# Optimization experiments

Hardware: AMD Instinct MI355X
Metric: run time of the kernel (lower is better)

Reference implementation:

```python
import jax, jax.numpy as jnp
import numpy as np

N, E, C, H, DE, B = 50000, 400000, 64, 4, 16, 64
EPS = 1e-5
NEG_SLOPE = 0.2
NBLOCKS = 2


def setup_inputs() -> dict:
    key = jax.random.key(0)
    ks = jax.random.split(key, 8)
    x = jax.random.normal(ks[0], (N, C), jnp.float32)
    edge_index = jax.random.randint(ks[1], (2, E), 0, N, dtype=jnp.int64)
    edge_attr = jax.random.normal(ks[2], (E, DE), jnp.float32)
    batch = jnp.sort(jax.random.randint(ks[3], (N,), 0, B, dtype=jnp.int64))
    s = 1.0 / np.sqrt(C)
    # stacked params for the 2 blocks
    Wl = jax.random.normal(ks[4], (NBLOCKS, C, H * C), jnp.float32) * s
    Wr = jax.random.normal(ks[5], (NBLOCKS, C, H * C), jnp.float32) * s
    We = jax.random.normal(ks[6], (NBLOCKS, DE, H * C), jnp.float32) * (1.0 / np.sqrt(DE))
    att = jax.random.normal(ks[7], (NBLOCKS, H, C), jnp.float32) * s
    gat_bias = jnp.zeros((NBLOCKS, C), jnp.float32)
    gn_weight = jnp.ones((NBLOCKS, C), jnp.float32)
    gn_bias = jnp.zeros((NBLOCKS, C), jnp.float32)
    gn_mean_scale = jnp.ones((NBLOCKS, C), jnp.float32)
    return dict(x=x, edge_index=edge_index, edge_attr=edge_attr, batch=batch,
                Wl=Wl, Wr=Wr, We=We, att=att, gat_bias=gat_bias,
                gn_weight=gn_weight, gn_bias=gn_bias, gn_mean_scale=gn_mean_scale)


def _segment_mean(v, seg, num):
    s = jax.ops.segment_sum(v, seg, num_segments=num)
    cnt = jax.ops.segment_sum(jnp.ones((v.shape[0], 1), v.dtype), seg, num_segments=num)
    return s / jnp.maximum(cnt, 1.0)


def _graph_norm(x, batch, w, b, ms):
    mean = _segment_mean(x, batch, B)                 # [B, C]
    sub = x - ms * mean[batch]
    var = _segment_mean(sub * sub, batch, B)          # [B, C]
    return sub / jnp.sqrt(var[batch] + EPS) * w + b


def _gatv2(x, src, dst, ea, Wl, Wr, We, att, bias):
    # src/dst/ea already include self loops (E2 = E + N edges)
    xl = (x @ Wl).reshape(N, H, C)                    # source transform
    xr = (x @ Wr).reshape(N, H, C)                    # target transform
    ee = (ea @ We).reshape(-1, H, C)                  # [E2, H, C]
    f = jax.nn.leaky_relu(xl[src] + xr[dst] + ee, NEG_SLOPE)
    logits = jnp.einsum('ehc,hc->eh', f, att)         # [E2, H]
    m = jax.ops.segment_max(logits, dst, num_segments=N)
    a = jnp.exp(logits - m[dst])
    denom = jax.ops.segment_sum(a, dst, num_segments=N)
    alpha = a / denom[dst]                            # per-target softmax
    out = jax.ops.segment_sum(xl[src] * alpha[:, :, None], dst, num_segments=N)
    return out.mean(axis=1) + bias                    # concat=False -> head mean


def reference(x, edge_index, edge_attr, batch, Wl, Wr, We, att, gat_bias,
              gn_weight, gn_bias, gn_mean_scale):
    loop = jnp.arange(N, dtype=edge_index.dtype)
    src = jnp.concatenate([edge_index[0], loop])
    dst = jnp.concatenate([edge_index[1], loop])
    # add_self_loops with fill_value='mean'
    ea = jnp.concatenate([edge_attr,
                          jnp.broadcast_to(edge_attr.mean(axis=0), (N, DE))])
    residual = x
    for i in range(NBLOCKS):
        h = _graph_norm(x, batch, gn_weight[i], gn_bias[i], gn_mean_scale[i])
        h = jax.nn.relu(h)
        x = _gatv2(h, src, dst, ea, Wl[i], Wr[i], We[i], att[i], gat_bias[i])
    return x + residual
```

## Files before the change

### kernel.cpp

```cpp
#include <hip/hip_runtime.h>
#include <math.h>

#define NN 50000
#define EE 400000
#define ETOT 450000
#define CC 64
#define HH 4
#define DEA 16
#define NBATCH 64
#define HC 256
#define EPSV 1e-5f
#define NB 49
#define NGB 782
#define NPW 2
#define HISTB 1758
#define PACKB 128

typedef unsigned short ushort_t;
typedef unsigned int uint_t;
using h2t = decltype(__builtin_amdgcn_cvt_pkrtz(0.0f, 0.0f));

__device__ __forceinline__ float4 ld4(const float* p){ return *(const float4*)p; }
__device__ __forceinline__ int rfl(int v){ return __builtin_amdgcn_readfirstlane(v); }
__device__ __forceinline__ ushort_t f2b(float f){
  uint_t u = __float_as_uint(f);
  uint_t r = (u + 0x7FFFu + ((u >> 16) & 1u)) >> 16;
  return (ushort_t)r;
}
__device__ __forceinline__ float b2f_lo(uint_t u){ return __uint_as_float(u << 16); }
__device__ __forceinline__ float b2f_hi(uint_t u){ return __uint_as_float(u & 0xFFFF0000u); }
__device__ __forceinline__ uint_t h2u(h2t h){ return __builtin_bit_cast(uint_t, h); }
__device__ __forceinline__ h2t u2h(uint_t u){ return __builtin_bit_cast(h2t, u); }

template<int CTRL>
__device__ __forceinline__ float dpp_add(float x){
  int y = __builtin_amdgcn_update_dpp(0, __float_as_int(x), CTRL, 0xF, 0xF, true);
  return x + __int_as_float(y);
}
__device__ __forceinline__ float red16(float x){
  x = dpp_add<0xB1>(x);
  x = dpp_add<0x4E>(x);
  x = dpp_add<0x141>(x);
  x = dpp_add<0x140>(x);
  return x;
}

__global__ __launch_bounds__(256)
void k_pre1(const float* __restrict__ ea, const int* __restrict__ dst,
            float* __restrict__ easum, int* __restrict__ cnt){
  int tid = threadIdx.x;
  int bid = blockIdx.x;
  int e = bid*256 + tid;
  if (e < ETOT){
    int d = (e < EE) ? dst[e] : (e - EE);
    atomicAdd(&cnt[d], 1);
  }
  if (bid < 1024){
    int gid = bid*256 + tid;
    const int gsz = 262144;
    float s = 0.f;
    for (long long i = gid; i < (long long)EE*DEA; i += gsz) s += ea[i];
    __shared__ float sd[256];
    sd[tid] = s; __syncthreads();
    if (tid < DEA){
      float t = 0.f;
      for (int j = tid; j < 256; j += DEA) t += sd[j];
      atomicAdd(&easum[tid], t);
    }
  }
}

__global__ __launch_bounds__(1024)
void k_scan1(const int* __restrict__ cnt, int* __restrict__ loc, int* __restrict__ bsum){
  __shared__ int wsum[16];
  int tid = threadIdx.x, lane = tid & 63, wv = tid >> 6;
  int i = blockIdx.x*1024 + tid;
  int v = (i < NN) ? cnt[i] : 0;
  int incl = v;
  #pragma unroll
  for (int off = 1; off < 64; off <<= 1){
    int t = __shfl_up(incl, off, 64);
    if (lane >= off) incl += t;
  }
  if (lane == 63) wsum[wv] = incl;
  __syncthreads();
  if (wv == 0){
    int s = (lane < 16) ? wsum[lane] : 0;
    #pragma unroll
    for (int off = 1; off < 16; off <<= 1){
      int t = __shfl_up(s, off, 64);
      if (lane >= off) s += t;
    }
    if (lane < 16) wsum[lane] = s;
  }
  __syncthreads();
  int excl = (wv ? wsum[wv-1] : 0) + incl - v;
  if (i < NN) loc[i] = excl;
  if (tid == 1023) bsum[blockIdx.x] = wsum[15];
}

__global__ void k_scan2(int* __restrict__ bsum, int* __restrict__ row_ptr){
  int lane = threadIdx.x;
  int v = (lane < NB) ? bsum[lane] : 0;
  int incl = v;
  #pragma unroll
  for (int off = 1; off < 64; off <<= 1){
    int t = __shfl_up(incl, off, 64);
    if (lane >= off) incl += t;
  }
  if (lane < NB) bsum[lane] = incl - v;
  if (lane == 63) row_ptr[NN] = incl;
}

__global__ __launch_bounds__(1024)
void k_scan3(const int* __restrict__ loc, const int* __restrict__ bsum,
             int* __restrict__ row_ptr, int* __restrict__ wp){
  int i = blockIdx.x*1024 + threadIdx.x;
  if (i < NN){
    int v = loc[i] + bsum[blockIdx.x];
    row_ptr[i] = v; wp[i] = v;
  }
}

__global__ __launch_bounds__(256)
void k_pre2(const int* __restrict__ dst, const int* __restrict__ src,
            const float* __restrict__ ea, const float* __restrict__ easum,
            int* __restrict__ wp, int* __restrict__ csrc, uint_t* __restrict__ eas,
            const float* __restrict__ Wl, const float* __restrict__ Wr,
            uint_t* __restrict__ Wq){
  int bid = blockIdx.x;
  int tid = threadIdx.x;
  if (bid < HISTB){
    int e = bid*256 + tid;
    if (e >= ETOT) return;
    int d, s;
    if (e < EE){ d = dst[e]; s = src[e]; } else { d = e - EE; s = d; }
    int pos = atomicAdd(&wp[d], 1);
    csrc[pos] = s;
    float buf[16];
    if (e < EE){
      #pragma unroll
      for (int q = 0; q < 4; q++){
        float4 v = ld4(ea + (size_t)e*DEA + q*4);
        buf[q*4+0]=v.x; buf[q*4+1]=v.y; buf[q*4+2]=v.z; buf[q*4+3]=v.w;
      }
    } else {
      const float invE = 1.0f / (float)EE;
      #pragma unroll
      for (int k = 0; k < 16; k++) buf[k] = easum[k]*invE;
    }
    uint_t pk[8];
    #pragma unroll
    for (int p = 0; p < 8; p++)
      pk[p] = h2u(__builtin_amdgcn_cvt_pkrtz(buf[2*p], buf[2*p+1]));
    *(uint4*)(eas + (size_t)pos*8 + 0) = make_uint4(pk[0], pk[1], pk[2], pk[3]);
    *(uint4*)(eas + (size_t)pos*8 + 4) = make_uint4(pk[4], pk[5], pk[6], pk[7]);
  } else {
    int t = (bid - HISTB)*256 + tid;
    int col = t & 255;
    int kp  = (t >> 8) & 31;
    int lm  = t >> 13;
    int l = lm >> 1, mat = lm & 1;
    const float* W = (mat ? Wr : Wl) + (size_t)l*CC*HC;
    float w0 = W[(size_t)(2*kp+0)*HC + col];
    float w1 = W[(size_t)(2*kp+1)*HC + col];
    Wq[(size_t)lm*8192 + kp*256 + col] = h2u(__builtin_amdgcn_cvt_pkrtz(w0, w1));
  }
}

__global__ __launch_bounds__(256)
void k_stats(const float* __restrict__ x, const int* __restrict__ batch,
             float* __restrict__ S, float* __restrict__ Q){
  int c = threadIdx.x & 63, g = threadIdx.x >> 6;
  int r0 = blockIdx.x*256;
  int hiR = r0 + 256; if (hiR > NN) hiR = NN;
  float s = 0.f, q = 0.f;
  int curb = -1;
  for (int n = r0 + g; n < hiR; n += 4){
    int b = batch[n];
    if (b != curb){
      if (curb >= 0){ atomicAdd(&S[curb*64+c], s); atomicAdd(&Q[curb*64+c], q); }
      curb = b; s = 0.f; q = 0.f;
    }
    float v = x[(size_t)n*CC + c];
    s += v; q += v*v;
  }
  if (curb >= 0){ atomicAdd(&S[curb*64+c], s); atomicAdd(&Q[curb*64+c], q); }
}

__device__ __forceinline__ int lowerb(const int* a, int n, int key){
  int lo = 0, hi = n;
  while (lo < hi){ int mid = (lo+hi) >> 1; if (a[mid] < key) lo = mid+1; else hi = mid; }
  return lo;
}

__global__ void k_fin(const float* __restrict__ S, const float* __restrict__ Q,
                      const int* __restrict__ batch,
                      const float* __restrict__ w, const float* __restrict__ bb,
                      const float* __restrict__ ms,
                      float* __restrict__ scale, float* __restrict__ shift){
  __shared__ float cntf;
  int b = blockIdx.x, c = threadIdx.x;
  if (c == 0){
    int lo = lowerb(batch, NN, b), hi = lowerb(batch, NN, b+1);
    cntf = fmaxf((float)(hi - lo), 1.f);
  }
  __syncthreads();
  float inv = 1.f / cntf;
  float m = S[b*64+c] * inv;
  float a = ms[c] * m;
  float var = Q[b*64+c]*inv - 2.f*a*m + a*a;
  var = fmaxf(var, 0.f);
  float rstd = rsqrtf(var + EPSV);
  float sc = rstd * w[c];
  scale[b*64+c] = sc;
  shift[b*64+c] = bb[c] - a*sc;
}

__global__ __launch_bounds__(256)
void k_gemm(const float* __restrict__ x, const int* __restrict__ batch,
            const float* __restrict__ scale, const float* __restrict__ shift,
            const uint_t* __restrict__ WqA, const uint_t* __restrict__ WqB,
            ushort_t* __restrict__ outA, ushort_t* __restrict__ outB){
  const uint_t* Wq = blockIdx.z ? WqB : WqA;
  ushort_t* out = blockIdx.z ? outB : outA;
  int n0 = blockIdx.x * 64;
  __shared__ uint_t hTp[32][72];
  int tid = threadIdx.x;
  for (int t = tid; t < 1024; t += 256){
    int r = t >> 4, ch = t & 15;
    int n = n0 + r;
    float4 v = make_float4(0.f,0.f,0.f,0.f);
    if (n < NN){
      int b = batch[n];
      v = ld4(x + (size_t)n*CC + ch*4);
      float4 sc = ld4(scale + b*64 + ch*4);
      float4 sh = ld4(shift + b*64 + ch*4);
      v.x = fmaxf(v.x*sc.x + sh.x, 0.f);
      v.y = fmaxf(v.y*sc.y + sh.y, 0.f);
      v.z = fmaxf(v.z*sc.z + sh.z, 0.f);
      v.w = fmaxf(v.w*sc.w + sh.w, 0.f);
    }
    hTp[ch*2+0][r] = h2u(__builtin_amdgcn_cvt_pkrtz(v.x, v.y));
    hTp[ch*2+1][r] = h2u(__builtin_amdgcn_cvt_pkrtz(v.z, v.w));
  }
  __syncthreads();
  int c = tid & 63, rg = tid >> 6;
  int r0 = rg * 16;
  float acc[16][4];
  #pragma unroll
  for (int i = 0; i < 16; i++){ acc[i][0]=0.f; acc[i][1]=0.f; acc[i][2]=0.f; acc[i][3]=0.f; }
  #pragma unroll 4
  for (int kp = 0; kp < 32; kp++){
    uint4 a0 = *(const uint4*)&hTp[kp][r0+0];
    uint4 a1 = *(const uint4*)&hTp[kp][r0+4];
    uint4 a2 = *(const uint4*)&hTp[kp][r0+8];
    uint4 a3 = *(const uint4*)&hTp[kp][r0+12];
    uint4 wv = *(const uint4*)(Wq + (size_t)kp*256 + c*4);
    h2t w0 = u2h(wv.x), w1 = u2h(wv.y), w2 = u2h(wv.z), w3 = u2h(wv.w);
    const uint_t av[16] = {a0.x,a0.y,a0.z,a0.w, a1.x,a1.y,a1.z,a1.w,
                           a2.x,a2.y,a2.z,a2.w, a3.x,a3.y,a3.z,a3.w};
    #pragma unroll
    for (int i = 0; i < 16; i++){
      h2t e = u2h(av[i]);
      acc[i][0] = __builtin_amdgcn_fdot2(e, w0, acc[i][0], false);
      acc[i][1] = __builtin_amdgcn_fdot2(e, w1, acc[i][1], false);
      acc[i][2] = __builtin_amdgcn_fdot2(e, w2, acc[i][2], false);
      acc[i][3] = __builtin_amdgcn_fdot2(e, w3, acc[i][3], false);
    }
  }
  #pragma unroll
  for (int i = 0; i < 16; i++){
    int n = n0 + r0 + i;
    if (n < NN){
      uint2 o;
      o.x = (uint_t)f2b(acc[i][0]) | ((uint_t)f2b(acc[i][1]) << 16);
      o.y = (uint_t)f2b(acc[i][2]) | ((uint_t)f2b(acc[i][3]) << 16);
      *(uint2*)(out + (size_t)n*HC + c*4) = o;
    }
  }
}

__global__ __launch_bounds__(256, 4)
void k_gat(const int* __restrict__ row_ptr, const int* __restrict__ csrc,
           const uint_t* __restrict__ eas,
           const ushort_t* __restrict__ xlh, const ushort_t* __restrict__ xrh,
           const float* __restrict__ We, const float* __restrict__ att,
           const float* __restrict__ bias, const float* __restrict__ resid,
           float* __restrict__ out){
  int lane = threadIdx.x & 63;
  int h = lane >> 4, cg = lane & 15;
  int col = h*64 + cg*4;
  int wid = (blockIdx.x*256 + threadIdx.x) >> 6;
  int n0 = wid * NPW;
  if (n0 >= NN) return;
  int n1 = n0 + NPW; if (n1 > NN) n1 = NN;

  uint_t werh[4][8];
  #pragma unroll
  for (int p = 0; p < 8; p++){
    float4 w0 = ld4(We + (size_t)(2*p+0)*HC + col);
    float4 w1 = ld4(We + (size_t)(2*p+1)*HC + col);
    werh[0][p] = h2u(__builtin_amdgcn_cvt_pkrtz(w0.x, w1.x));
    werh[1][p] = h2u(__builtin_amdgcn_cvt_pkrtz(w0.y, w1.y));
    werh[2][p] = h2u(__builtin_amdgcn_cvt_pkrtz(w0.z, w1.z));
    werh[3][p] = h2u(__builtin_amdgcn_cvt_pkrtz(w0.w, w1.w));
  }
  #pragma unroll
  for (int j = 0; j < 4; j++)
    #pragma unroll
    for (int p = 0; p < 8; p++)
      asm volatile("" : "+v"(werh[j][p]));

  float4 attv = ld4(att + col);
  float4 biasv = ld4(bias + cg*4);

  for (int n = n0; n < n1; n++){
    int rr0 = rfl(row_ptr[n]), rr1 = rfl(row_ptr[n+1]);
    uint2 xrp = *(const uint2*)(xrh + (size_t)n*HC + col);
    float xr0 = b2f_lo(xrp.x), xr1 = b2f_hi(xrp.x);
    float xr2 = b2f_lo(xrp.y), xr3 = b2f_hi(xrp.y);
    float m = -3.4e38f, dsum = 0.f;
    float a0 = 0.f, a1 = 0.f, a2 = 0.f, a3 = 0.f;

    int sC = rfl(csrc[rr0]);
    uint2 xlp = *(const uint2*)(xlh + (size_t)sC*HC + col);
    uint_t earC[8];
    {
      const uint_t* ep = eas + (size_t)rr0*8;
      #pragma unroll
      for (int p = 0; p < 8; p++) earC[p] = ep[p];
    }

    for (int idx = rr0; idx < rr1; idx++){
      int idn = (idx+1 < rr1) ? idx+1 : rr0;
      int sN = rfl(csrc[idn]);
      uint2 xlq = *(const uint2*)(xlh + (size_t)sN*HC + col);
      uint_t earN[8];
      {
        const uint_t* ep = eas + (size_t)rfl(idn)*8;
        #pragma unroll
        for (int p = 0; p < 8; p++) earN[p] = ep[p];
      }

      float xl0 = b2f_lo(xlp.x), xl1 = b2f_hi(xlp.x);
      float xl2 = b2f_lo(xlp.y), xl3 = b2f_hi(xlp.y);

      float p0 = 0.f, p1 = 0.f, p2 = 0.f, p3 = 0.f;
      #pragma unroll
      for (int p = 0; p < 8; p++){
        h2t e = u2h(earC[p]);
        p0 = __builtin_amdgcn_fdot2(e, u2h(werh[0][p]), p0, false);
        p1 = __builtin_amdgcn_fdot2(e, u2h(werh[1][p]), p1, false);
        p2 = __builtin_amdgcn_fdot2(e, u2h(werh[2][p]), p2, false);
        p3 = __builtin_amdgcn_fdot2(e, u2h(werh[3][p]), p3, false);
      }
      float v0 = xl0 + xr0 + p0; v0 = (v0 > 0.f) ? v0 : 0.2f*v0;
      float v1 = xl1 + xr1 + p1; v1 = (v1 > 0.f) ? v1 : 0.2f*v1;
      float v2 = xl2 + xr2 + p2; v2 = (v2 > 0.f) ? v2 : 0.2f*v2;
      float v3 = xl3 + xr3 + p3; v3 = (v3 > 0.f) ? v3 : 0.2f*v3;
      float pl = v0*attv.x + v1*attv.y + v2*attv.z + v3*attv.w;
      pl = red16(pl);

      float mn = fmaxf(m, pl);
      float sc = __expf(m - mn);
      float wexp = __expf(pl - mn);
      dsum = dsum*sc + wexp;
      a0 = a0*sc + wexp*xl0;
      a1 = a1*sc + wexp*xl1;
      a2 = a2*sc + wexp*xl2;
      a3 = a3*sc + wexp*xl3;
      m = mn;

      xlp = xlq;
      #pragma unroll
      for (int p = 0; p < 8; p++) earC[p] = earN[p];
    }

    float inv = 1.0f / dsum;
    float o0 = a0*inv, o1 = a1*inv, o2 = a2*inv, o3 = a3*inv;
    #pragma unroll
    for (int off = 16; off < 64; off <<= 1){
      o0 += __shfl_xor(o0, off, 64);
      o1 += __shfl_xor(o1, off, 64);
      o2 += __shfl_xor(o2, off, 64);
      o3 += __shfl_xor(o3, off, 64);
    }
    if (lane < 16){
      float r0v = o0*0.25f + biasv.x;
      float r1v = o1*0.25f + biasv.y;
      float r2v = o2*0.25f + biasv.z;
      float r3v = o3*0.25f + biasv.w;
      if (resid){
        float4 rv = ld4(resid + (size_t)n*CC + cg*4);
        r0v += rv.x; r1v += rv.y; r2v += rv.z; r3v += rv.w;
      }
      *(float4*)(out + (size_t)n*CC + cg*4) = make_float4(r0v, r1v, r2v, r3v);
    }
  }
}

extern "C" void kernel_launch(void* const* d_in, const int* in_sizes, int n_in,
                              void* d_out, int out_size, void* d_ws, size_t ws_size,
                              hipStream_t stream) {
  const float* x     = (const float*)d_in[0];
  const int*   ei    = (const int*)d_in[1];
  const int*   src   = ei;
  const int*   dst   = ei + EE;
  const float* ea    = (const float*)d_in[2];
  const int*   batch = (const int*)d_in[3];
  const float* Wl    = (const float*)d_in[4];
  const float* Wr    = (const float*)d_in[5];
  const float* We    = (const float*)d_in[6];
  const float* att   = (const float*)d_in[7];
  const float* gb    = (const float*)d_in[8];
  const float* gw    = (const float*)d_in[9];
  const float* gnb   = (const float*)d_in[10];
  const float* gms   = (const float*)d_in[11];
  float* out = (float*)d_out;

  char* ws = (char*)d_ws;
  size_t off = 0;
  auto alloc = [&](size_t bytes) -> void* {
    void* p = ws + off; off += (bytes + 255) & ~(size_t)255; return p;
  };
  int*   cnt     = (int*)alloc(NN*sizeof(int));
  float* easum   = (float*)alloc(64*sizeof(float));
  float* statSQ  = (float*)alloc(4*4096*sizeof(float));
  size_t zbytes  = off;
  int*   loc     = (int*)alloc(NN*sizeof(int));
  int*   bsum    = (int*)alloc(64*sizeof(int));
  int*   wp      = (int*)alloc(NN*sizeof(int));
  int*   row_ptr = (int*)alloc((NN+1)*sizeof(int));
  int*   csrc    = (int*)alloc((size_t)ETOT*sizeof(int));
  uint_t* eas    = (uint_t*)alloc((size_t)ETOT*8*sizeof(uint_t));
  float* scaleb  = (float*)alloc(4096*sizeof(float));
  float* shiftb  = (float*)alloc(4096*sizeof(float));
  uint_t* Wq     = (uint_t*)alloc((size_t)4*8192*sizeof(uint_t));
  ushort_t* xlh  = (ushort_t*)alloc((size_t)NN*HC*sizeof(ushort_t));
  ushort_t* xrh  = (ushort_t*)alloc((size_t)NN*HC*sizeof(ushort_t));
  float* xbuf    = (float*)alloc((size_t)NN*CC*sizeof(float));
  if (off > ws_size) return;

  hipMemsetAsync(cnt, 0, zbytes, stream);
  k_pre1<<<HISTB, 256, 0, stream>>>(ea, dst, easum, cnt);
  k_scan1<<<NB, 1024, 0, stream>>>(cnt, loc, bsum);
  k_scan2<<<1, 64, 0, stream>>>(bsum, row_ptr);
  k_scan3<<<NB, 1024, 0, stream>>>(loc, bsum, row_ptr, wp);
  k_pre2<<<HISTB + PACKB, 256, 0, stream>>>(dst, src, ea, easum, wp, csrc, eas, Wl, Wr, Wq);

  int gatBlocks = (NN + NPW*4 - 1) / (NPW*4);
  for (int i = 0; i < 2; i++){
    const float* xin = i ? xbuf : x;
    float* S = statSQ + i*4096;
    float* Q = statSQ + 2*4096 + i*4096;
    k_stats<<<(NN+255)/256, 256, 0, stream>>>(xin, batch, S, Q);
    k_fin<<<64, 64, 0, stream>>>(S, Q, batch, gw + i*CC, gnb + i*CC, gms + i*CC, scaleb, shiftb);
    k_gemm<<<dim3(NGB, 1, 2), 256, 0, stream>>>(xin, batch, scaleb, shiftb,
                                                Wq + (size_t)(i*2+0)*8192,
                                                Wq + (size_t)(i*2+1)*8192,
                                                xlh, xrh);
    k_gat<<<gatBlocks, 256, 0, stream>>>(row_ptr, csrc, eas, xlh, xrh,
                                         We + (size_t)i*DEA*HC, att + i*HH*CC,
                                         gb + i*CC, i ? x : nullptr, i ? out : xbuf);
  }
}
```

Baseline: 382.6 us.

## Fold first-block stats into preprocessing kernel and process two edges per GAT iteration

Moves the block-0 graph-norm statistics pass into the k_pre2 launch as extra blocks, which removes one kernel launch and lets that work overlap with the CSR build. The GAT edge loop now handles two edges per iteration. It prefetches two sources and two edge attributes ahead and merges both into the online softmax with a single rescale, aiming for more memory-level parallelism and fewer serial exp/reduction chains. The cost is higher register pressure from doubled prefetch buffers, plus wasted work on odd-degree rows.

```diff
diff --git a/kernel.cpp b/kernel.cpp
--- a/kernel.cpp
+++ b/kernel.cpp
@@ -15,6 +15,7 @@
 #define NPW 2
 #define HISTB 1758
 #define PACKB 128
+#define STATB 196
 
 typedef unsigned short ushort_t;
 typedef unsigned int uint_t;
@@ -127,7 +128,9 @@
             const float* __restrict__ ea, const float* __restrict__ easum,
             int* __restrict__ wp, int* __restrict__ csrc, uint_t* __restrict__ eas,
             const float* __restrict__ Wl, const float* __restrict__ Wr,
-            uint_t* __restrict__ Wq){
+            uint_t* __restrict__ Wq,
+            const float* __restrict__ x, const int* __restrict__ batch,
+            float* __restrict__ S, float* __restrict__ Q){
   int bid = blockIdx.x;
   int tid = threadIdx.x;
   if (bid < HISTB){
@@ -155,7 +158,7 @@
       pk[p] = h2u(__builtin_amdgcn_cvt_pkrtz(buf[2*p], buf[2*p+1]));
     *(uint4*)(eas + (size_t)pos*8 + 0) = make_uint4(pk[0], pk[1], pk[2], pk[3]);
     *(uint4*)(eas + (size_t)pos*8 + 4) = make_uint4(pk[4], pk[5], pk[6], pk[7]);
-  } else {
+  } else if (bid < HISTB + PACKB){
     int t = (bid - HISTB)*256 + tid;
     int col = t & 255;
     int kp  = (t >> 8) & 31;
@@ -165,6 +168,22 @@
     float w0 = W[(size_t)(2*kp+0)*HC + col];
     float w1 = W[(size_t)(2*kp+1)*HC + col];
     Wq[(size_t)lm*8192 + kp*256 + col] = h2u(__builtin_amdgcn_cvt_pkrtz(w0, w1));
+  } else {
+    int c = tid & 63, g = tid >> 6;
+    int r0 = (bid - HISTB - PACKB)*256;
+    int hiR = r0 + 256; if (hiR > NN) hiR = NN;
+    float s = 0.f, q = 0.f;
+    int curb = -1;
+    for (int n = r0 + g; n < hiR; n += 4){
+      int b = batch[n];
+      if (b != curb){
+        if (curb >= 0){ atomicAdd(&S[curb*64+c], s); atomicAdd(&Q[curb*64+c], q); }
+        curb = b; s = 0.f; q = 0.f;
+      }
+      float v = x[(size_t)n*CC + c];
+      s += v; q += v*v;
+    }
+    if (curb >= 0){ atomicAdd(&S[curb*64+c], s); atomicAdd(&Q[curb*64+c], q); }
   }
 }
 
@@ -323,58 +342,81 @@
     float m = -3.4e38f, dsum = 0.f;
     float a0 = 0.f, a1 = 0.f, a2 = 0.f, a3 = 0.f;
 
-    int sC = rfl(csrc[rr0]);
-    uint2 xlp = *(const uint2*)(xlh + (size_t)sC*HC + col);
-    uint_t earC[8];
+    int i1c = (rr0+1 < rr1) ? rr0+1 : rr0;
+    int sA = rfl(csrc[rr0]);
+    int sB = rfl(csrc[i1c]);
+    uint2 xA = *(const uint2*)(xlh + (size_t)sA*HC + col);
+    uint2 xB = *(const uint2*)(xlh + (size_t)sB*HC + col);
+    uint_t eaA[8], eaB[8];
     {
-      const uint_t* ep = eas + (size_t)rr0*8;
+      const uint_t* p0 = eas + (size_t)rr0*8;
+      const uint_t* p1 = eas + (size_t)i1c*8;
       #pragma unroll
-      for (int p = 0; p < 8; p++) earC[p] = ep[p];
-    }
-
-    for (int idx = rr0; idx < rr1; idx++){
-      int idn = (idx+1 < rr1) ? idx+1 : rr0;
-      int sN = rfl(csrc[idn]);
-      uint2 xlq = *(const uint2*)(xlh + (size_t)sN*HC + col);
-      uint_t earN[8];
+      for (int p = 0; p < 8; p++){ eaA[p] = p0[p]; eaB[p] = p1[p]; }
+    }
+
+    for (int idx = rr0; idx < rr1; idx += 2){
+      int j0 = (idx+2 < rr1) ? idx+2 : rr0;
+      int j1 = (idx+3 < rr1) ? idx+3 : rr0;
+      int tA = rfl(csrc[j0]);
+      int tB = rfl(csrc[j1]);
+      uint2 xC = *(const uint2*)(xlh + (size_t)tA*HC + col);
+      uint2 xD = *(const uint2*)(xlh + (size_t)tB*HC + col);
+      uint_t eaC[8], eaD[8];
       {
-        const uint_t* ep = eas + (size_t)rfl(idn)*8;
+        const uint_t* p0 = eas + (size_t)j0*8;
+        const uint_t* p1 = eas + (size_t)j1*8;
         #pragma unroll
-        for (int p = 0; p < 8; p++) earN[p] = ep[p];
+        for (int p = 0; p < 8; p++){ eaC[p] = p0[p]; eaD[p] = p1[p]; }
       }
 
-      float xl0 = b2f_lo(xlp.x), xl1 = b2f_hi(xlp.x);
-      float xl2 = b2f_lo(xlp.y), xl3 = b2f_hi(xlp.y);
-
-      float p0 = 0.f, p1 = 0.f, p2 = 0.f, p3 = 0.f;
+      float xl00 = b2f_lo(xA.x), xl01 = b2f_hi(xA.x);
+      float xl02 = b2f_lo(xA.y), xl03 = b2f_hi(xA.y);
+      float xl10 = b2f_lo(xB.x), xl11 = b2f_hi(xB.x);
+      float xl12 = b2f_lo(xB.y), xl13 = b2f_hi(xB.y);
+
+      float p00=0.f,p01=0.f,p02=0.f,p03=0.f, p10=0.f,p11=0.f,p12=0.f,p13=0.f;
       #pragma unroll
       for (int p = 0; p < 8; p++){
-        h2t e = u2h(earC[p]);
-        p0 = __builtin_amdgcn_fdot2(e, u2h(werh[0][p]), p0, false);
-        p1 = __builtin_amdgcn_fdot2(e, u2h(werh[1][p]), p1, false);
-        p2 = __builtin_amdgcn_fdot2(e, u2h(werh[2][p]), p2, false);
-        p3 = __builtin_amdgcn_fdot2(e, u2h(werh[3][p]), p3, false);
+        h2t e0 = u2h(eaA[p]);
+        h2t e1 = u2h(eaB[p]);
+        p00 = __builtin_amdgcn_fdot2(e0, u2h(werh[0][p]), p00, false);
+        p10 = __builtin_amdgcn_fdot2(e1, u2h(werh[0][p]), p10, false);
+        p01 = __builtin_amdgcn_fdot2(e0, u2h(werh[1][p]), p01, false);
+        p11 = __builtin_amdgcn_fdot2(e1, u2h(werh[1][p]), p11, false);
+        p02 = __builtin_amdgcn_fdot2(e0, u2h(werh[2][p]), p02, false);
+        p12 = __builtin_amdgcn_fdot2(e1, u2h(werh[2][p]), p12, false);
+        p03 = __builtin_amdgcn_fdot2(e0, u2h(werh[3][p]), p03, false);
+        p13 = __builtin_amdgcn_fdot2(e1, u2h(werh[3][p]), p13, false);
       }
-      float v0 = xl0 + xr0 + p0; v0 = (v0 > 0.f) ? v0 : 0.2f*v0;
-      float v1 = xl1 + xr1 + p1; v1 = (v1 > 0.f) ? v1 : 0.2f*v1;
-      float v2 = xl2 + xr2 + p2; v2 = (v2 > 0.f) ? v2 : 0.2f*v2;
-      float v3 = xl3 + xr3 + p3; v3 = (v3 > 0.f) ? v3 : 0.2f*v3;
-      float pl = v0*attv.x + v1*attv.y + v2*attv.z + v3*attv.w;
-      pl = red16(pl);
-
-      float mn = fmaxf(m, pl);
+      float u00 = xl00 + xr0 + p00; u00 = (u00 > 0.f) ? u00 : 0.2f*u00;
+      float u01 = xl01 + xr1 + p01; u01 = (u01 > 0.f) ? u01 : 0.2f*u01;
+      float u02 = xl02 + xr2 + p02; u02 = (u02 > 0.f) ? u02 : 0.2f*u02;
+      float u03 = xl03 + xr3 + p03; u03 = (u03 > 0.f) ? u03 : 0.2f*u03;
+      float u10 = xl10 + xr0 + p10; u10 = (u10 > 0.f) ? u10 : 0.2f*u10;
+      float u11 = xl11 + xr1 + p11; u11 = (u11 > 0.f) ? u11 : 0.2f*u11;
+      float u12 = xl12 + xr2 + p12; u12 = (u12 > 0.f) ? u12 : 0.2f*u12;
+      float u13 = xl13 + xr3 + p13; u13 = (u13 > 0.f) ? u13 : 0.2f*u13;
+      float pl0 = u00*attv.x + u01*attv.y + u02*attv.z + u03*attv.w;
+      float pl1 = u10*attv.x + u11*attv.y + u12*attv.z + u13*attv.w;
+      pl0 = red16(pl0);
+      pl1 = red16(pl1);
+      if (idx + 1 >= rr1) pl1 = -3.4e38f;
+
+      float mn = fmaxf(fmaxf(m, pl0), pl1);
       float sc = __expf(m - mn);
-      float wexp = __expf(pl - mn);
-      dsum = dsum*sc + wexp;
-      a0 = a0*sc + wexp*xl0;
-      a1 = a1*sc + wexp*xl1;
-      a2 = a2*sc + wexp*xl2;
-      a3 = a3*sc + wexp*xl3;
+      float w0 = __expf(pl0 - mn);
+      float w1 = __expf(pl1 - mn);
+      dsum = dsum*sc + w0 + w1;
+      a0 = a0*sc + w0*xl00 + w1*xl10;
+      a1 = a1*sc + w0*xl01 + w1*xl11;
+      a2 = a2*sc + w0*xl02 + w1*xl12;
+      a3 = a3*sc + w0*xl03 + w1*xl13;
       m = mn;
 
-      xlp = xlq;
+      xA = xC; xB = xD;
       #pragma unroll
-      for (int p = 0; p < 8; p++) earC[p] = earN[p];
+      for (int p = 0; p < 8; p++){ eaA[p] = eaC[p]; eaB[p] = eaD[p]; }
     }
 
     float inv = 1.0f / dsum;
@@ -447,14 +489,16 @@
   k_scan1<<<NB, 1024, 0, stream>>>(cnt, loc, bsum);
   k_scan2<<<1, 64, 0, stream>>>(bsum, row_ptr);
   k_scan3<<<NB, 1024, 0, stream>>>(loc, bsum, row_ptr, wp);
-  k_pre2<<<HISTB + PACKB, 256, 0, stream>>>(dst, src, ea, easum, wp, csrc, eas, Wl, Wr, Wq);
+  k_pre2<<<HISTB + PACKB + STATB, 256, 0, stream>>>(dst, src, ea, easum, wp, csrc, eas,
+                                                    Wl, Wr, Wq, x, batch,
+                                                    statSQ + 0, statSQ + 2*4096);
 
   int gatBlocks = (NN + NPW*4 - 1) / (NPW*4);
   for (int i = 0; i < 2; i++){
     const float* xin = i ? xbuf : x;
     float* S = statSQ + i*4096;
     float* Q = statSQ + 2*4096 + i*4096;
-    k_stats<<<(NN+255)/256, 256, 0, stream>>>(xin, batch, S, Q);
+    if (i) k_stats<<<(NN+255)/256, 256, 0, stream>>>(xin, batch, S, Q);
     k_fin<<<64, 64, 0, stream>>>(S, Q, batch, gw + i*CC, gnb + i*CC, gms + i*CC, scaleb, shiftb);
     k_gemm<<<dim3(NGB, 1, 2), 256, 0, stream>>>(xin, batch, scaleb, shiftb,
                                                 Wq + (size_t)(i*2+0)*8192,
```

New measurement: 373.5 us (median of 2 runs). 1.02x faster.
